# Optimization experiments

Hardware: AMD Instinct MI355X
Metric: run time of the kernel (lower is better)

The kernel has to match this reference:

```python
import jax, jax.numpy as jnp
import numpy as np

N_NODES = 100000
N_EDGES = 3200000
NUM_GRAPHS = 1024
F_IN = 128
EMB = 32
N_HIDDEN_LAYERS = 3  # conv_layers list; initial_conv is separate


def setup_inputs() -> dict:
    key = jax.random.key(0)
    ks = jax.random.split(key, 10)
    x = jax.random.normal(ks[0], (N_NODES, F_IN), dtype=jnp.float32)
    edge_index = jax.random.randint(ks[1], (2, N_EDGES), 0, N_NODES, dtype=jnp.int64)
    batch_index = jnp.sort(jax.random.randint(ks[2], (N_NODES,), 0, NUM_GRAPHS, dtype=jnp.int64))
    # GCNConv params: lin weight [in, out] + bias [out]
    W0 = jax.random.normal(ks[3], (F_IN, EMB), dtype=jnp.float32) * (1.0 / np.sqrt(F_IN))
    b0 = jnp.zeros((EMB,), dtype=jnp.float32)
    Ws = jax.random.normal(ks[4], (N_HIDDEN_LAYERS, EMB, EMB), dtype=jnp.float32) * (1.0 / np.sqrt(EMB))
    bs = jnp.zeros((N_HIDDEN_LAYERS, EMB), dtype=jnp.float32)
    Wout = jax.random.normal(ks[5], (EMB, 1), dtype=jnp.float32) * (1.0 / np.sqrt(EMB))
    bout = jnp.zeros((1,), dtype=jnp.float32)
    return {"x": x, "edge_index": edge_index, "batch_index": batch_index,
            "W0": W0, "b0": b0, "Ws": Ws, "bs": bs, "Wout": Wout, "bout": bout}


def _gcn_conv(h, W, b, src, dst, norm):
    # x @ W, then degree-normalized scatter-add aggregation (source -> target), then bias
    h = h @ W                                            # [N, out]
    msg = h[src] * norm[:, None]                         # gather + scale, [E+N, out]
    agg = jax.ops.segment_sum(msg, dst, num_segments=N_NODES)
    return agg + b


def reference(x, edge_index, batch_index, W0, b0, Ws, bs, Wout, bout):
    loops = jnp.arange(N_NODES, dtype=edge_index.dtype)
    src = jnp.concatenate([edge_index[0], loops])        # self-loops appended (PyG default)
    dst = jnp.concatenate([edge_index[1], loops])
    deg = jax.ops.segment_sum(jnp.ones_like(dst, dtype=x.dtype), dst, num_segments=N_NODES)
    dinv = jax.lax.rsqrt(jnp.maximum(deg, 1.0))          # deg >= 1 due to self-loops
    norm = dinv[src] * dinv[dst]                         # symmetric normalization

    h = jax.nn.leaky_relu(_gcn_conv(x, W0, b0, src, dst, norm), 0.01)
    for i in range(N_HIDDEN_LAYERS):
        h = jax.nn.leaky_relu(_gcn_conv(h, Ws[i], bs[i], src, dst, norm), 0.01)

    pooled = jax.ops.segment_max(h, batch_index, num_segments=NUM_GRAPHS)  # global max pool
    out = pooled @ Wout + bout                           # [NUM_GRAPHS, 1]
    return out, pooled
```

## Files before the change

kernel.cpp:

```cpp
#include <hip/hip_runtime.h>

#define N_NODES   100000
#define N_EDGES   3200000
#define NUM_GRAPHS 1024
#define F_IN      128
#define EMB       32

#define NRANGE    4
#define RANGE_SZ  25000
#define NKEY      (N_NODES * NRANGE)

#define NGROUP    256
#define GROUP_SZ  391
#define BCAP      13824
#define FB        1024
#define FILL_ITER 14

#define PART_TILE 8192
#define PART_THREADS 512
#define PART_NB   ((N_EDGES + PART_TILE - 1) / PART_TILE)

__global__ void init_k(int* __restrict__ bucketCnt, int* __restrict__ rp2) {
    int i = threadIdx.x;
    if (i < NGROUP) bucketCnt[i] = 0;
    if (i == 0) rp2[NKEY] = N_EDGES;
}

__global__ __launch_bounds__(PART_THREADS) void partition_k(const int* __restrict__ src,
                                                            const int* __restrict__ dst,
                                                            int* __restrict__ bucketCnt,
                                                            unsigned* __restrict__ bEdges) {
    __shared__ unsigned stage[PART_TILE];
    __shared__ unsigned char bucketOf[PART_TILE];
    __shared__ int hist[NGROUP];
    __shared__ int lbase[NGROUP + 1];
    __shared__ int gbase[NGROUP];
    __shared__ int sc[NGROUP];
    int t = threadIdx.x;
    int base = blockIdx.x * PART_TILE;
    for (int k = t; k < NGROUP; k += PART_THREADS) hist[k] = 0;
    __syncthreads();
    unsigned val[16]; int bk[16], rk[16];
#pragma unroll
    for (int i = 0; i < 16; ++i) {
        int e = base + i * PART_THREADS + t;
        bk[i] = -1;
        if (e < N_EDGES) {
            unsigned s = (unsigned)__builtin_nontemporal_load(src + e);
            unsigned d = (unsigned)__builtin_nontemporal_load(dst + e);
            int b = (int)(d / GROUP_SZ);
            val[i] = ((d - (unsigned)b * GROUP_SZ) << 17) | s;
            bk[i] = b;
            rk[i] = atomicAdd(&hist[b], 1);
        }
    }
    __syncthreads();
    if (t < NGROUP) sc[t] = hist[t];
    __syncthreads();
    for (int off = 1; off < NGROUP; off <<= 1) {
        int v = 0;
        if (t < NGROUP) v = sc[t] + ((t >= off) ? sc[t - off] : 0);
        __syncthreads();
        if (t < NGROUP) sc[t] = v;
        __syncthreads();
    }
    if (t < NGROUP) {
        lbase[t] = sc[t] - hist[t];
        if (hist[t] > 0) gbase[t] = atomicAdd(&bucketCnt[t], hist[t]);
        if (t == NGROUP - 1) lbase[NGROUP] = sc[t];
    }
    __syncthreads();
#pragma unroll
    for (int i = 0; i < 16; ++i)
        if (bk[i] >= 0) {
            int j = lbase[bk[i]] + rk[i];
            stage[j] = val[i];
            bucketOf[j] = (unsigned char)bk[i];
        }
    __syncthreads();
    int total = lbase[NGROUP];
    for (int j = t; j < total; j += PART_THREADS) {
        int b = bucketOf[j];
        int off = gbase[b] + (j - lbase[b]);
        if (off < BCAP) __builtin_nontemporal_store(stage[j], &bEdges[(size_t)b * BCAP + off]);
    }
}

__global__ __launch_bounds__(256) void bucketbase_k(const int* __restrict__ bucketCnt,
                                                    int* __restrict__ bucketBase) {
    __shared__ int l[256];
    int t = threadIdx.x;
    int c = bucketCnt[t]; if (c > BCAP) c = BCAP;
    l[t] = c;
    __syncthreads();
    for (int off = 1; off < 256; off <<= 1) {
        int v = l[t] + ((t >= off) ? l[t - off] : 0);
        __syncthreads();
        l[t] = v;
        __syncthreads();
    }
    bucketBase[t] = l[t] - c;
}

__global__ __launch_bounds__(FB) void fill_k(const unsigned* __restrict__ bEdges,
                                             const int* __restrict__ bucketCnt,
                                             const int* __restrict__ bucketBase,
                                             int* __restrict__ rp2,
                                             float* __restrict__ dinv,
                                             int* __restrict__ col) {
    __shared__ int cur[GROUP_SZ * 4];
    __shared__ int nodesum[512];
    __shared__ unsigned lout[BCAP];
    int b = blockIdx.x, t = threadIdx.x;
    int colBase = bucketBase[b];

    int nb = N_NODES - b * GROUP_SZ; if (nb > GROUP_SZ) nb = GROUP_SZ;
    int nk = nb * 4;
    for (int k = t; k < nk; k += FB) cur[k] = 0;
    __syncthreads();

    int cnt = bucketCnt[b]; if (cnt > BCAP) cnt = BCAP;
    const unsigned* be = bEdges + (size_t)b * BCAP;
    unsigned val[FILL_ITER];
#pragma unroll
    for (int i = 0; i < FILL_ITER; ++i) {
        int idx = i * FB + t;
        val[i] = 0xFFFFFFFFu;
        if (idx < cnt) {
            unsigned v = __builtin_nontemporal_load(be + idx);
            val[i] = v;
            unsigned key = (v >> 17) * NRANGE + (v & 0x1FFFFu) / RANGE_SZ;
            atomicAdd(&cur[key], 1);
        }
    }
    __syncthreads();

    int h0 = 0, h1 = 0, h2 = 0, h3 = 0;
    if (t < nb) {
        h0 = cur[t * 4]; h1 = cur[t * 4 + 1]; h2 = cur[t * 4 + 2]; h3 = cur[t * 4 + 3];
        int dsum = h0 + h1 + h2 + h3;
        nodesum[t] = dsum;
        dinv[b * GROUP_SZ + t] = rsqrtf((float)(dsum + 1));
    } else if (t < 512) nodesum[t] = 0;
    __syncthreads();
    for (int off = 1; off < 512; off <<= 1) {
        int v = 0;
        if (t < 512) v = nodesum[t] + ((t >= off) ? nodesum[t - off] : 0);
        __syncthreads();
        if (t < 512) nodesum[t] = v;
        __syncthreads();
    }
    if (t < nb) {
        int p0 = (t > 0) ? nodesum[t - 1] : 0;
        int p1 = p0 + h0, p2 = p1 + h1, p3 = p2 + h2;
        int kb = (b * GROUP_SZ + t) * 4;
        int4 w; w.x = colBase + p0; w.y = colBase + p1; w.z = colBase + p2; w.w = colBase + p3;
        *(int4*)(rp2 + kb) = w;
        cur[t * 4] = p0; cur[t * 4 + 1] = p1; cur[t * 4 + 2] = p2; cur[t * 4 + 3] = p3;
    }
    __syncthreads();

#pragma unroll
    for (int i = 0; i < FILL_ITER; ++i) {
        unsigned v = val[i];
        if (v != 0xFFFFFFFFu) {
            unsigned key = (v >> 17) * NRANGE + (v & 0x1FFFFu) / RANGE_SZ;
            int slot = atomicAdd(&cur[key], 1);
            lout[slot] = v & 0x1FFFFu;
        }
    }
    __syncthreads();

    for (int i = t; i < cnt; i += FB)
        __builtin_nontemporal_store((int)lout[i], col + colBase + i);
}

__global__ __launch_bounds__(256) void transform0_k(const float* __restrict__ x,
                                                    const float* __restrict__ W0,
                                                    const float* __restrict__ dinv,
                                                    float4* __restrict__ tmp4) {
    int i = blockIdx.x * blockDim.x + threadIdx.x;
    if (i >= (N_NODES / 8) * 8) return;
    int gid = i >> 3, q = i & 7;
    int n0 = gid * 8;
    const float* wq = W0 + q * 4;
    float4 acc[8];
#pragma unroll
    for (int j = 0; j < 8; ++j) acc[j] = make_float4(0.f, 0.f, 0.f, 0.f);
#pragma unroll 2
    for (int kc = 0; kc < F_IN / 4; ++kc) {
        float4 w0 = *(const float4*)(wq + (kc * 4 + 0) * EMB);
        float4 w1 = *(const float4*)(wq + (kc * 4 + 1) * EMB);
        float4 w2 = *(const float4*)(wq + (kc * 4 + 2) * EMB);
        float4 w3 = *(const float4*)(wq + (kc * 4 + 3) * EMB);
#pragma unroll
        for (int j = 0; j < 8; ++j) {
            float4 xv = *(const float4*)(x + (long long)(n0 + j) * F_IN + kc * 4);
            acc[j].x += xv.x * w0.x; acc[j].y += xv.x * w0.y; acc[j].z += xv.x * w0.z; acc[j].w += xv.x * w0.w;
            acc[j].x += xv.y * w1.x; acc[j].y += xv.y * w1.y; acc[j].z += xv.y * w1.z; acc[j].w += xv.y * w1.w;
            acc[j].x += xv.z * w2.x; acc[j].y += xv.z * w2.y; acc[j].z += xv.z * w2.z; acc[j].w += xv.z * w2.w;
            acc[j].x += xv.w * w3.x; acc[j].y += xv.w * w3.y; acc[j].z += xv.w * w3.z; acc[j].w += xv.w * w3.w;
        }
    }
#pragma unroll
    for (int j = 0; j < 8; ++j) {
        float dn = dinv[n0 + j];
        acc[j].x *= dn; acc[j].y *= dn; acc[j].z *= dn; acc[j].w *= dn;
        tmp4[(n0 + j) * 8 + q] = acc[j];
    }
}

template <bool FUSE>
__global__ __launch_bounds__(256) void gather_k(const int* __restrict__ rp2,
                                                const int* __restrict__ col,
                                                const float4* __restrict__ tmp4,
                                                const float* __restrict__ dinv,
                                                const float* __restrict__ bias,
                                                const float* __restrict__ W,
                                                float4* __restrict__ out4) {
    __shared__ float4 Wl[256];
    __shared__ float4 hx[32 * 9];
    int t = threadIdx.x;
    int i = blockIdx.x * 256 + t;
    int n = i >> 3, q = i & 7, ln = t >> 3;
    if (FUSE) {
        Wl[t] = ((const float4*)W)[t];
        __syncthreads();
    }

    int4 rpv = *(const int4*)(rp2 + n * 4);
    int rp4  = rp2[n * 4 + 4];
    int begs[5] = {rpv.x, rpv.y, rpv.z, rpv.w, rp4};

    float4 acc = tmp4[i];
#pragma unroll
    for (int r = 0; r < NRANGE; ++r) {
        int k = begs[r], end = begs[r + 1];
        for (; k < end && (k & 3); ++k) {
            float4 v = tmp4[col[k] * 8 + q];
            acc.x += v.x; acc.y += v.y; acc.z += v.z; acc.w += v.w;
        }
        for (; k + 4 <= end; k += 4) {
            int4 c0 = *(const int4*)(col + k);
            float4 v0 = tmp4[c0.x * 8 + q], v1 = tmp4[c0.y * 8 + q];
            float4 v2 = tmp4[c0.z * 8 + q], v3 = tmp4[c0.w * 8 + q];
            acc.x += (v0.x + v1.x) + (v2.x + v3.x);
            acc.y += (v0.y + v1.y) + (v2.y + v3.y);
            acc.z += (v0.z + v1.z) + (v2.z + v3.z);
            acc.w += (v0.w + v1.w) + (v2.w + v3.w);
        }
        for (; k < end; ++k) {
            float4 v = tmp4[col[k] * 8 + q];
            acc.x += v.x; acc.y += v.y; acc.z += v.z; acc.w += v.w;
        }
    }
    float dn = dinv[n];
    float4 bb = ((const float4*)bias)[q];
    float4 rr;
    rr.x = acc.x * dn + bb.x;
    rr.y = acc.y * dn + bb.y;
    rr.z = acc.z * dn + bb.z;
    rr.w = acc.w * dn + bb.w;
    rr.x = rr.x > 0.f ? rr.x : 0.01f * rr.x;
    rr.y = rr.y > 0.f ? rr.y : 0.01f * rr.y;
    rr.z = rr.z > 0.f ? rr.z : 0.01f * rr.z;
    rr.w = rr.w > 0.f ? rr.w : 0.01f * rr.w;

    if (!FUSE) {
        out4[i] = rr;
        return;
    }
    hx[ln * 9 + q] = rr;
    __builtin_amdgcn_wave_barrier();
    float4 tq = make_float4(0.f, 0.f, 0.f, 0.f);
#pragma unroll
    for (int kq = 0; kq < 8; ++kq) {
        float4 hv = hx[ln * 9 + kq];
        float4 w0 = Wl[(kq * 4 + 0) * 8 + q];
        float4 w1 = Wl[(kq * 4 + 1) * 8 + q];
        float4 w2 = Wl[(kq * 4 + 2) * 8 + q];
        float4 w3 = Wl[(kq * 4 + 3) * 8 + q];
        tq.x += hv.x * w0.x; tq.y += hv.x * w0.y; tq.z += hv.x * w0.z; tq.w += hv.x * w0.w;
        tq.x += hv.y * w1.x; tq.y += hv.y * w1.y; tq.z += hv.y * w1.z; tq.w += hv.y * w1.w;
        tq.x += hv.z * w2.x; tq.y += hv.z * w2.y; tq.z += hv.z * w2.z; tq.w += hv.z * w2.w;
        tq.x += hv.w * w3.x; tq.y += hv.w * w3.y; tq.z += hv.w * w3.z; tq.w += hv.w * w3.w;
    }
    tq.x *= dn; tq.y *= dn; tq.z *= dn; tq.w *= dn;
    out4[i] = tq;
}

__global__ __launch_bounds__(256) void pool_head_k(const float* __restrict__ h,
                                                   const int* __restrict__ batch,
                                                   const float* __restrict__ Wout,
                                                   const float* __restrict__ bout,
                                                   float* __restrict__ out) {
    int g = blockIdx.x;
    __shared__ int sbeg, send;
    if (threadIdx.x == 0) {
        int lo = 0, hi = N_NODES;
        while (lo < hi) { int mid = (lo + hi) >> 1; if (batch[mid] < g) lo = mid + 1; else hi = mid; }
        sbeg = lo;
        hi = N_NODES;
        while (lo < hi) { int mid = (lo + hi) >> 1; if (batch[mid] < g + 1) lo = mid + 1; else hi = mid; }
        send = lo;
    }
    __syncthreads();
    int beg = sbeg, end = send;
    int t = threadIdx.x, c = t & 31, r = t >> 5;
    float m = -INFINITY;
    for (int n = beg + r; n < end; n += 8) m = fmaxf(m, h[n * EMB + c]);
    __shared__ float red[256];
    red[t] = m;
    __syncthreads();
    if (t < 128) red[t] = fmaxf(red[t], red[t + 128]);
    __syncthreads();
    if (t < 64) red[t] = fmaxf(red[t], red[t + 64]);
    __syncthreads();
    if (t < 32) {
        m = fmaxf(red[t], red[t + 32]);
        out[NUM_GRAPHS + g * EMB + c] = m;
        float p = m * Wout[c];
#pragma unroll
        for (int o = 16; o > 0; o >>= 1) p += __shfl_xor(p, o, 32);
        if (c == 0) out[g] = p + bout[0];
    }
}

extern "C" void kernel_launch(void* const* d_in, const int* in_sizes, int n_in,
                              void* d_out, int out_size, void* d_ws, size_t ws_size,
                              hipStream_t stream) {
    const float* x     = (const float*)d_in[0];
    const int*   ei    = (const int*)d_in[1];
    const int*   src   = ei;
    const int*   dst   = ei + N_EDGES;
    const int*   batch = (const int*)d_in[2];
    const float* W0    = (const float*)d_in[3];
    const float* b0    = (const float*)d_in[4];
    const float* Ws    = (const float*)d_in[5];
    const float* bs    = (const float*)d_in[6];
    const float* Wout  = (const float*)d_in[7];
    const float* bout  = (const float*)d_in[8];
    float* out = (float*)d_out;

    char* ws = (char*)d_ws;
    int*   rp2       = (int*)ws;   ws += (size_t)(NKEY + 4) * 4;
    int*   col       = (int*)ws;   ws += (size_t)N_EDGES * 4;
    float* dinv      = (float*)ws; ws += (size_t)N_NODES * 4;
    float* tmp       = (float*)ws; ws += (size_t)N_NODES * EMB * 4;
    float* h         = (float*)ws; ws += (size_t)N_NODES * EMB * 4;
    int*   bucketCnt = (int*)ws;   ws += 1024;
    int*   bucketBase= (int*)ws;   ws += 1024;
    unsigned* bEdges = (unsigned*)tmp;

    const int B = 256;
    const int G8_g = (N_NODES * 8) / B;
    const int T_g  = (N_NODES + B - 1) / B;

    init_k<<<1, B, 0, stream>>>(bucketCnt, rp2);
    partition_k<<<PART_NB, PART_THREADS, 0, stream>>>(src, dst, bucketCnt, bEdges);
    bucketbase_k<<<1, 256, 0, stream>>>(bucketCnt, bucketBase);
    fill_k<<<NGROUP, FB, 0, stream>>>(bEdges, bucketCnt, bucketBase, rp2, dinv, col);

    transform0_k<<<T_g, B, 0, stream>>>(x, W0, dinv, (float4*)tmp);
    gather_k<true ><<<G8_g, B, 0, stream>>>(rp2, col, (const float4*)tmp, dinv, b0,           Ws + 0 * 1024, (float4*)h);
    gather_k<true ><<<G8_g, B, 0, stream>>>(rp2, col, (const float4*)h,   dinv, bs + 0 * EMB, Ws + 1 * 1024, (float4*)tmp);
    gather_k<true ><<<G8_g, B, 0, stream>>>(rp2, col, (const float4*)tmp, dinv, bs + 1 * EMB, Ws + 2 * 1024, (float4*)h);
    gather_k<false><<<G8_g, B, 0, stream>>>(rp2, col, (const float4*)h,   dinv, bs + 2 * EMB, nullptr,       (float4*)tmp);

    pool_head_k<<<NUM_GRAPHS, B, 0, stream>>>(tmp, batch, Wout, bout, out);
}
```

Baseline: 447.5 us.

## Process multiple node tiles per block with column indices staged in LDS

```diff
diff --git a/kernel.cpp b/kernel.cpp
--- a/kernel.cpp
+++ b/kernel.cpp
@@ -19,6 +19,11 @@
 #define PART_TILE 8192
 #define PART_THREADS 512
 #define PART_NB   ((N_EDGES + PART_TILE - 1) / PART_TILE)
+
+#define NTILE     3125
+#define NBLK      1024
+#define TMAX      4
+#define LCAP      1408
 
 __global__ void init_k(int* __restrict__ bucketCnt, int* __restrict__ rp2) {
     int i = threadIdx.x;
@@ -211,82 +216,171 @@
 }
 
 template <bool FUSE>
-__global__ __launch_bounds__(256) void gather_k(const int* __restrict__ rp2,
-                                                const int* __restrict__ col,
-                                                const float4* __restrict__ tmp4,
-                                                const float* __restrict__ dinv,
-                                                const float* __restrict__ bias,
-                                                const float* __restrict__ W,
-                                                float4* __restrict__ out4) {
+__global__ __launch_bounds__(256, 4) void gather_mt_k(const int* __restrict__ rp2,
+                                                      const int* __restrict__ col,
+                                                      const float4* __restrict__ inb,
+                                                      const float* __restrict__ dinv,
+                                                      const float* __restrict__ bias,
+                                                      const float* __restrict__ W,
+                                                      float4* __restrict__ outb) {
     __shared__ float4 Wl[256];
     __shared__ float4 hx[32 * 9];
+    __shared__ int colS[TMAX * LCAP];
+    __shared__ int begsS[TMAX][32][5];
+
     int t = threadIdx.x;
-    int i = blockIdx.x * 256 + t;
-    int n = i >> 3, q = i & 7, ln = t >> 3;
-    if (FUSE) {
-        Wl[t] = ((const float4*)W)[t];
-        __syncthreads();
-    }
-
-    int4 rpv = *(const int4*)(rp2 + n * 4);
-    int rp4  = rp2[n * 4 + 4];
-    int begs[5] = {rpv.x, rpv.y, rpv.z, rpv.w, rp4};
-
-    float4 acc = tmp4[i];
-#pragma unroll
+    int blk = blockIdx.x;
+    int q = t & 7, ln = t >> 3;
+
+    if (FUSE) Wl[t] = ((const float4*)W)[t];
+
+    int inLmask = 0;
+#pragma unroll
+    for (int tt = 0; tt < TMAX; ++tt) {
+        int tile = blk + tt * NBLK;
+        if (tile >= NTILE) continue;
+        int S = rp2[tile * 128];
+        int E = rp2[tile * 128 + 128];
+        int span = E - S;
+        int inL = (span <= LCAP) ? 1 : 0;
+        inLmask |= inL << tt;
+        if (t < 160) {
+            int node = t / 5, r = t % 5;
+            int v = rp2[tile * 128 + node * 4 + r];
+            begsS[tt][node][r] = inL ? (v - S) : v;
+        }
+        if (inL)
+            for (int j = t; j < span; j += 256)
+                colS[tt * LCAP + j] = __builtin_nontemporal_load(col + S + j);
+    }
+    __syncthreads();
+
+    float4 acc[TMAX];
+#pragma unroll
+    for (int tt = 0; tt < TMAX; ++tt) {
+        int tile = blk + tt * NBLK;
+        acc[tt] = (tile < NTILE) ? inb[tile * 256 + t]
+                                 : make_float4(0.f, 0.f, 0.f, 0.f);
+    }
+
+#pragma unroll 1
     for (int r = 0; r < NRANGE; ++r) {
-        int k = begs[r], end = begs[r + 1];
-        for (; k < end && (k & 3); ++k) {
-            float4 v = tmp4[col[k] * 8 + q];
-            acc.x += v.x; acc.y += v.y; acc.z += v.z; acc.w += v.w;
-        }
-        for (; k + 4 <= end; k += 4) {
-            int4 c0 = *(const int4*)(col + k);
-            float4 v0 = tmp4[c0.x * 8 + q], v1 = tmp4[c0.y * 8 + q];
-            float4 v2 = tmp4[c0.z * 8 + q], v3 = tmp4[c0.w * 8 + q];
-            acc.x += (v0.x + v1.x) + (v2.x + v3.x);
-            acc.y += (v0.y + v1.y) + (v2.y + v3.y);
-            acc.z += (v0.z + v1.z) + (v2.z + v3.z);
-            acc.w += (v0.w + v1.w) + (v2.w + v3.w);
-        }
-        for (; k < end; ++k) {
-            float4 v = tmp4[col[k] * 8 + q];
-            acc.x += v.x; acc.y += v.y; acc.z += v.z; acc.w += v.w;
-        }
-    }
-    float dn = dinv[n];
-    float4 bb = ((const float4*)bias)[q];
-    float4 rr;
-    rr.x = acc.x * dn + bb.x;
-    rr.y = acc.y * dn + bb.y;
-    rr.z = acc.z * dn + bb.z;
-    rr.w = acc.w * dn + bb.w;
-    rr.x = rr.x > 0.f ? rr.x : 0.01f * rr.x;
-    rr.y = rr.y > 0.f ? rr.y : 0.01f * rr.y;
-    rr.z = rr.z > 0.f ? rr.z : 0.01f * rr.z;
-    rr.w = rr.w > 0.f ? rr.w : 0.01f * rr.w;
-
-    if (!FUSE) {
-        out4[i] = rr;
-        return;
-    }
-    hx[ln * 9 + q] = rr;
-    __builtin_amdgcn_wave_barrier();
-    float4 tq = make_float4(0.f, 0.f, 0.f, 0.f);
-#pragma unroll
-    for (int kq = 0; kq < 8; ++kq) {
-        float4 hv = hx[ln * 9 + kq];
-        float4 w0 = Wl[(kq * 4 + 0) * 8 + q];
-        float4 w1 = Wl[(kq * 4 + 1) * 8 + q];
-        float4 w2 = Wl[(kq * 4 + 2) * 8 + q];
-        float4 w3 = Wl[(kq * 4 + 3) * 8 + q];
-        tq.x += hv.x * w0.x; tq.y += hv.x * w0.y; tq.z += hv.x * w0.z; tq.w += hv.x * w0.w;
-        tq.x += hv.y * w1.x; tq.y += hv.y * w1.y; tq.z += hv.y * w1.z; tq.w += hv.y * w1.w;
-        tq.x += hv.z * w2.x; tq.y += hv.z * w2.y; tq.z += hv.z * w2.z; tq.w += hv.z * w2.w;
-        tq.x += hv.w * w3.x; tq.y += hv.w * w3.y; tq.z += hv.w * w3.z; tq.w += hv.w * w3.w;
-    }
-    tq.x *= dn; tq.y *= dn; tq.z *= dn; tq.w *= dn;
-    out4[i] = tq;
+#pragma unroll
+        for (int tt = 0; tt < TMAX; ++tt) {
+            int tile = blk + tt * NBLK;
+            if (tile >= NTILE) continue;
+            int k = begsS[tt][ln][r], end = begsS[tt][ln][r + 1];
+            float4 a = acc[tt];
+            if ((inLmask >> tt) & 1) {
+                const int* cS = &colS[tt * LCAP];
+                for (; k + 8 <= end; k += 8) {
+                    int c0 = cS[k], c1 = cS[k + 1], c2 = cS[k + 2], c3 = cS[k + 3];
+                    int c4 = cS[k + 4], c5 = cS[k + 5], c6 = cS[k + 6], c7 = cS[k + 7];
+                    float4 v0 = inb[c0 * 8 + q], v1 = inb[c1 * 8 + q];
+                    float4 v2 = inb[c2 * 8 + q], v3 = inb[c3 * 8 + q];
+                    float4 v4 = inb[c4 * 8 + q], v5 = inb[c5 * 8 + q];
+                    float4 v6 = inb[c6 * 8 + q], v7 = inb[c7 * 8 + q];
+                    a.x += (v0.x + v1.x) + (v2.x + v3.x);
+                    a.y += (v0.y + v1.y) + (v2.y + v3.y);
+                    a.z += (v0.z + v1.z) + (v2.z + v3.z);
+                    a.w += (v0.w + v1.w) + (v2.w + v3.w);
+                    a.x += (v4.x + v5.x) + (v6.x + v7.x);
+                    a.y += (v4.y + v5.y) + (v6.y + v7.y);
+                    a.z += (v4.z + v5.z) + (v6.z + v7.z);
+                    a.w += (v4.w + v5.w) + (v6.w + v7.w);
+                }
+                if (k + 4 <= end) {
+                    int c0 = cS[k], c1 = cS[k + 1], c2 = cS[k + 2], c3 = cS[k + 3];
+                    float4 v0 = inb[c0 * 8 + q], v1 = inb[c1 * 8 + q];
+                    float4 v2 = inb[c2 * 8 + q], v3 = inb[c3 * 8 + q];
+                    a.x += (v0.x + v1.x) + (v2.x + v3.x);
+                    a.y += (v0.y + v1.y) + (v2.y + v3.y);
+                    a.z += (v0.z + v1.z) + (v2.z + v3.z);
+                    a.w += (v0.w + v1.w) + (v2.w + v3.w);
+                    k += 4;
+                }
+                if (k < end) {
+                    int e1 = end - 1;
+                    int i1 = min(k + 1, e1), i2 = min(k + 2, e1), i3 = min(k + 3, e1);
+                    float m1 = (k + 1 < end) ? 1.f : 0.f;
+                    float m2 = (k + 2 < end) ? 1.f : 0.f;
+                    float m3 = (k + 3 < end) ? 1.f : 0.f;
+                    int c0 = cS[k], c1 = cS[i1], c2 = cS[i2], c3 = cS[i3];
+                    float4 v0 = inb[c0 * 8 + q], v1 = inb[c1 * 8 + q];
+                    float4 v2 = inb[c2 * 8 + q], v3 = inb[c3 * 8 + q];
+                    a.x += (v0.x + m1 * v1.x) + (m2 * v2.x + m3 * v3.x);
+                    a.y += (v0.y + m1 * v1.y) + (m2 * v2.y + m3 * v3.y);
+                    a.z += (v0.z + m1 * v1.z) + (m2 * v2.z + m3 * v3.z);
+                    a.w += (v0.w + m1 * v1.w) + (m2 * v2.w + m3 * v3.w);
+                }
+            } else {
+                for (; k + 4 <= end; k += 4) {
+                    int c0 = col[k], c1 = col[k + 1], c2 = col[k + 2], c3 = col[k + 3];
+                    float4 v0 = inb[c0 * 8 + q], v1 = inb[c1 * 8 + q];
+                    float4 v2 = inb[c2 * 8 + q], v3 = inb[c3 * 8 + q];
+                    a.x += (v0.x + v1.x) + (v2.x + v3.x);
+                    a.y += (v0.y + v1.y) + (v2.y + v3.y);
+                    a.z += (v0.z + v1.z) + (v2.z + v3.z);
+                    a.w += (v0.w + v1.w) + (v2.w + v3.w);
+                }
+                if (k < end) {
+                    int e1 = end - 1;
+                    int i1 = min(k + 1, e1), i2 = min(k + 2, e1), i3 = min(k + 3, e1);
+                    float m1 = (k + 1 < end) ? 1.f : 0.f;
+                    float m2 = (k + 2 < end) ? 1.f : 0.f;
+                    float m3 = (k + 3 < end) ? 1.f : 0.f;
+                    int c0 = col[k], c1 = col[i1], c2 = col[i2], c3 = col[i3];
+                    float4 v0 = inb[c0 * 8 + q], v1 = inb[c1 * 8 + q];
+                    float4 v2 = inb[c2 * 8 + q], v3 = inb[c3 * 8 + q];
+                    a.x += (v0.x + m1 * v1.x) + (m2 * v2.x + m3 * v3.x);
+                    a.y += (v0.y + m1 * v1.y) + (m2 * v2.y + m3 * v3.y);
+                    a.z += (v0.z + m1 * v1.z) + (m2 * v2.z + m3 * v3.z);
+                    a.w += (v0.w + m1 * v1.w) + (m2 * v2.w + m3 * v3.w);
+                }
+            }
+            acc[tt] = a;
+        }
+    }
+
+#pragma unroll
+    for (int tt = 0; tt < TMAX; ++tt) {
+        int tile = blk + tt * NBLK;
+        if (tile >= NTILE) continue;
+        int n = tile * 32 + ln;
+        float dn = dinv[n];
+        float4 bb = ((const float4*)bias)[q];
+        float4 rr;
+        rr.x = acc[tt].x * dn + bb.x;
+        rr.y = acc[tt].y * dn + bb.y;
+        rr.z = acc[tt].z * dn + bb.z;
+        rr.w = acc[tt].w * dn + bb.w;
+        rr.x = rr.x > 0.f ? rr.x : 0.01f * rr.x;
+        rr.y = rr.y > 0.f ? rr.y : 0.01f * rr.y;
+        rr.z = rr.z > 0.f ? rr.z : 0.01f * rr.z;
+        rr.w = rr.w > 0.f ? rr.w : 0.01f * rr.w;
+        if (FUSE) {
+            __builtin_amdgcn_wave_barrier();
+            hx[ln * 9 + q] = rr;
+            __builtin_amdgcn_wave_barrier();
+            float4 tq = make_float4(0.f, 0.f, 0.f, 0.f);
+#pragma unroll
+            for (int kq = 0; kq < 8; ++kq) {
+                float4 hv = hx[ln * 9 + kq];
+                float4 w0 = Wl[(kq * 4 + 0) * 8 + q];
+                float4 w1 = Wl[(kq * 4 + 1) * 8 + q];
+                float4 w2 = Wl[(kq * 4 + 2) * 8 + q];
+                float4 w3 = Wl[(kq * 4 + 3) * 8 + q];
+                tq.x += hv.x * w0.x; tq.y += hv.x * w0.y; tq.z += hv.x * w0.z; tq.w += hv.x * w0.w;
+                tq.x += hv.y * w1.x; tq.y += hv.y * w1.y; tq.z += hv.y * w1.z; tq.w += hv.y * w1.w;
+                tq.x += hv.z * w2.x; tq.y += hv.z * w2.y; tq.z += hv.z * w2.z; tq.w += hv.z * w2.w;
+                tq.x += hv.w * w3.x; tq.y += hv.w * w3.y; tq.z += hv.w * w3.z; tq.w += hv.w * w3.w;
+            }
+            tq.x *= dn; tq.y *= dn; tq.z *= dn; tq.w *= dn;
+            outb[tile * 256 + t] = tq;
+        } else {
+            outb[tile * 256 + t] = rr;
+        }
+    }
 }
 
 __global__ __launch_bounds__(256) void pool_head_k(const float* __restrict__ h,
@@ -353,7 +447,6 @@
     unsigned* bEdges = (unsigned*)tmp;
 
     const int B = 256;
-    const int G8_g = (N_NODES * 8) / B;
     const int T_g  = (N_NODES + B - 1) / B;
 
     init_k<<<1, B, 0, stream>>>(bucketCnt, rp2);
@@ -362,10 +455,11 @@
     fill_k<<<NGROUP, FB, 0, stream>>>(bEdges, bucketCnt, bucketBase, rp2, dinv, col);
 
     transform0_k<<<T_g, B, 0, stream>>>(x, W0, dinv, (float4*)tmp);
-    gather_k<true ><<<G8_g, B, 0, stream>>>(rp2, col, (const float4*)tmp, dinv, b0,           Ws + 0 * 1024, (float4*)h);
-    gather_k<true ><<<G8_g, B, 0, stream>>>(rp2, col, (const float4*)h,   dinv, bs + 0 * EMB, Ws + 1 * 1024, (float4*)tmp);
-    gather_k<true ><<<G8_g, B, 0, stream>>>(rp2, col, (const float4*)tmp, dinv, bs + 1 * EMB, Ws + 2 * 1024, (float4*)h);
-    gather_k<false><<<G8_g, B, 0, stream>>>(rp2, col, (const float4*)h,   dinv, bs + 2 * EMB, nullptr,       (float4*)tmp);
+
+    gather_mt_k<true ><<<NBLK, B, 0, stream>>>(rp2, col, (const float4*)tmp, dinv, b0,           Ws + 0 * 1024, (float4*)h);
+    gather_mt_k<true ><<<NBLK, B, 0, stream>>>(rp2, col, (const float4*)h,   dinv, bs + 0 * EMB, Ws + 1 * 1024, (float4*)tmp);
+    gather_mt_k<true ><<<NBLK, B, 0, stream>>>(rp2, col, (const float4*)tmp, dinv, bs + 1 * EMB, Ws + 2 * 1024, (float4*)h);
+    gather_mt_k<false><<<NBLK, B, 0, stream>>>(rp2, col, (const float4*)h,   dinv, bs + 2 * EMB, nullptr,       (float4*)tmp);
 
     pool_head_k<<<NUM_GRAPHS, B, 0, stream>>>(tmp, batch, Wout, bout, out);
 }
```

New measurement: 424.2 us. 1.05x faster.
